# Optimization experiments

Measured on AMD Instinct MI355X. Metric: run time of the kernel, lower is better.

## Reference

```python
import jax, jax.numpy as jnp
import numpy as np

N_NODES = 100000


def _gcn_norm(edge_index, num_nodes):
    # PyG GCNConv default: add self-loops, symmetric normalization.
    src = jnp.concatenate([edge_index[0], jnp.arange(num_nodes, dtype=edge_index.dtype)])
    dst = jnp.concatenate([edge_index[1], jnp.arange(num_nodes, dtype=edge_index.dtype)])
    deg = jax.ops.segment_sum(jnp.ones_like(dst, dtype=jnp.float32), dst, num_segments=num_nodes)
    dis = jnp.where(deg > 0, jax.lax.rsqrt(deg), 0.0)  # deg^{-1/2}
    norm = dis[src] * dis[dst]  # [E + N]
    return src, dst, norm


def _gcn_conv(x, W, b, src, dst, norm, num_nodes):
    h = x @ W.T                      # [N, out] transform first (out < in)
    msg = h[src] * norm[:, None]     # gather + per-edge scale
    agg = jax.ops.segment_sum(msg, dst, num_segments=num_nodes)  # scatter-add
    return agg + b


def setup_inputs() -> dict:
    key = jax.random.key(0)
    ks = jax.random.split(key, 12)
    E = 3200000
    x = jax.random.normal(ks[0], (N_NODES, 128), dtype=jnp.float32)
    edge_index = jax.random.randint(ks[1], (2, E), 0, N_NODES, dtype=jnp.int64)
    s = lambda k, sh, fan: jax.random.normal(k, sh, dtype=jnp.float32) * (1.0 / np.sqrt(fan))
    return {
        "x": x,
        "edge_index": edge_index,
        "W1": s(ks[2], (32, 128), 128), "b1": jnp.zeros((32,), jnp.float32),
        "W2": s(ks[3], (16, 32), 32),   "b2": jnp.zeros((16,), jnp.float32),
        "w_ih": s(ks[4], (32, 16), 16), "w_hh": s(ks[5], (32, 8), 8),
        "b_ih": s(ks[6], (32,), 8),     "b_hh": s(ks[7], (32,), 8),
        "W_out": s(ks[8], (1, 8), 8),   "b_out": jnp.zeros((1,), jnp.float32),
    }


def reference(x, edge_index, W1, b1, W2, b2, w_ih, w_hh, b_ih, b_hh, W_out, b_out):
    src, dst, norm = _gcn_norm(edge_index, N_NODES)
    h = jax.nn.relu(_gcn_conv(x, W1, b1, src, dst, norm, N_NODES))   # [N, 32]
    h = jax.nn.relu(_gcn_conv(h, W2, b2, src, dst, norm, N_NODES))   # [N, 16]
    # Single-timestep LSTM with h0 = c0 = 0 (gate order: i, f, g, o).
    gates = h @ w_ih.T + b_ih + b_hh   # [N, 32]; h0 @ w_hh.T term is zero
    i, f, g, o = jnp.split(gates, 4, axis=-1)
    c = jax.nn.sigmoid(i) * jnp.tanh(g)
    hh = jax.nn.sigmoid(o) * jnp.tanh(c)  # [N, 8]
    out = hh @ W_out.T + b_out            # [N, 1]
    return out.squeeze(-1)                # [N]
```

## Files before the change

kernel.cpp:

```cpp
#include <hip/hip_runtime.h>
#include <hip/hip_fp16.h>
#include <math.h>

static constexpr int N = 100000;
static constexpr int SHIFT = 7;
static constexpr int BUCKN = 1 << SHIFT;
static constexpr int NBUCK = (N + BUCKN - 1) >> SHIFT;
static constexpr int CHUNK = 12288;
static constexpr int STRIDE = 5120;

__global__ __launch_bounds__(1024) void k_init(int* __restrict__ gcur) {
    int b = threadIdx.x;
    if (b < NBUCK) gcur[b] = b * STRIDE;
}

__global__ __launch_bounds__(1024) void k_part(const int* __restrict__ src,
                                               const int* __restrict__ dst,
                                               int* __restrict__ gcur,
                                               int* __restrict__ col, int E) {
    __shared__ int ss[CHUNK];
    __shared__ int ds[CHUNK];
    __shared__ int hl[NBUCK];
    __shared__ int cur[NBUCK];
    const int t = threadIdx.x, b = blockIdx.x;
    if (t < NBUCK) hl[t] = 0;
    __syncthreads();
    const int e0 = b * CHUNK;
    const int m = min(CHUNK, E - e0);
    for (int i = t; i < m; i += 1024) {
        int d = dst[e0 + i], s = src[e0 + i];
        ss[i] = s;
        ds[i] = d;
        atomicAdd(&hl[d >> SHIFT], 1);
    }
    __syncthreads();
    if (t < NBUCK) cur[t] = atomicAdd(&gcur[t], hl[t]);
    __syncthreads();
    for (int i = t; i < m; i += 1024) {
        int d = ds[i];
        int pos = atomicAdd(&cur[d >> SHIFT], 1);
        col[pos] = ss[i] | ((d & (BUCKN - 1)) << 17);
    }
}

__global__ __launch_bounds__(1024) void k_sort(const int* __restrict__ gcur,
                                               int* __restrict__ col,
                                               int* __restrict__ deg,
                                               int* __restrict__ row_start) {
    __shared__ int es[STRIDE];
    __shared__ int cnt[BUCKN];
    __shared__ int cur[BUCKN];
    const int t = threadIdx.x, buck = blockIdx.x;
    const int s0 = buck * STRIDE;
    int n = gcur[buck] - s0;
    if (n > STRIDE) n = STRIDE;
    if (t < BUCKN) cnt[t] = 0;
    __syncthreads();
    for (int i = t; i < n; i += 1024) {
        int p = col[s0 + i];
        es[i] = p;
        atomicAdd(&cnt[(p >> 17) & (BUCKN - 1)], 1);
    }
    __syncthreads();
    if (t < BUCKN) cur[t] = cnt[t];
    __syncthreads();
    for (int off = 1; off < BUCKN; off <<= 1) {
        int v = (t < BUCKN && t >= off) ? cur[t - off] : 0;
        __syncthreads();
        if (t < BUCKN) cur[t] += v;
        __syncthreads();
    }
    if (t < BUCKN) {
        int excl = cur[t] - cnt[t];
        int node = buck * BUCKN + t;
        if (node < N) {
            deg[node] = cnt[t];
            row_start[node] = s0 + excl;
        }
        cur[t] = excl;
    }
    __syncthreads();
    for (int i = t; i < n; i += 1024) {
        int p = es[i];
        int pos = atomicAdd(&cur[(p >> 17) & (BUCKN - 1)], 1);
        col[s0 + pos] = p & 0x1FFFF;
    }
}

__global__ __launch_bounds__(256) void k_xw1(
        const float* __restrict__ x, const float* __restrict__ W1,
        const int* __restrict__ deg, __half* __restrict__ g1h) {
    __shared__ float4 wtv[32 * 33];
    __shared__ float4 xsv[1024];
    const int t = threadIdx.x;
    const float4* W1v = (const float4*)W1;
    for (int idx = t; idx < 1024; idx += 256) {
        int j = idx >> 5, kb = idx & 31;
        wtv[kb * 33 + j] = W1v[idx];
    }
    const float4* x4 = (const float4*)x + (size_t)blockIdx.x * 1024;
    for (int idx = t; idx < 1024; idx += 256) xsv[idx] = x4[idx];
    __syncthreads();

    const int j = t & 31, ng = t >> 5;
    float a0 = 0.f, a1 = 0.f, a2 = 0.f, a3 = 0.f;
#pragma unroll 4
    for (int kb = 0; kb < 32; ++kb) {
        float4 w = wtv[kb * 33 + j];
        float4 x0 = xsv[(4 * ng + 0) * 32 + kb];
        float4 x1 = xsv[(4 * ng + 1) * 32 + kb];
        float4 x2 = xsv[(4 * ng + 2) * 32 + kb];
        float4 x3 = xsv[(4 * ng + 3) * 32 + kb];
        a0 = fmaf(w.x, x0.x, fmaf(w.y, x0.y, fmaf(w.z, x0.z, fmaf(w.w, x0.w, a0))));
        a1 = fmaf(w.x, x1.x, fmaf(w.y, x1.y, fmaf(w.z, x1.z, fmaf(w.w, x1.w, a1))));
        a2 = fmaf(w.x, x2.x, fmaf(w.y, x2.y, fmaf(w.z, x2.z, fmaf(w.w, x2.w, a2))));
        a3 = fmaf(w.x, x3.x, fmaf(w.y, x3.y, fmaf(w.z, x3.z, fmaf(w.w, x3.w, a3))));
    }
    const int nb = blockIdx.x * 32 + 4 * ng;
    g1h[(nb + 0) * 32 + j] = __float2half(a0 * rsqrtf((float)(deg[nb + 0] + 1)));
    g1h[(nb + 1) * 32 + j] = __float2half(a1 * rsqrtf((float)(deg[nb + 1] + 1)));
    g1h[(nb + 2) * 32 + j] = __float2half(a2 * rsqrtf((float)(deg[nb + 2] + 1)));
    g1h[(nb + 3) * 32 + j] = __float2half(a3 * rsqrtf((float)(deg[nb + 3] + 1)));
}

__global__ __launch_bounds__(256) void k_gather1(
        const int* __restrict__ row_start, const int* __restrict__ deg,
        const int* __restrict__ col, const __half* __restrict__ g1h,
        const float* __restrict__ b1, float* __restrict__ h1) {
    const int t = threadIdx.x;
    const int lane = t & 63, w = t >> 6;
    const int q = lane & 3;
    const int node = blockIdx.x * 64 + w * 16 + (lane >> 2);
    const int nc = node < N ? node : N - 1;
    const int rs = row_start[nc];
    const int ne = (node < N) ? deg[nc] : 0;
    const uint4* g1v = (const uint4*)g1h;

    float acc[8];
    {
        uint4 rv = g1v[nc * 4 + q];
        const __half2* hp = (const __half2*)&rv;
#pragma unroll
        for (int m2 = 0; m2 < 4; ++m2) {
            float2 f = __half22float2(hp[m2]);
            acc[2 * m2] = f.x;
            acc[2 * m2 + 1] = f.y;
        }
    }
    for (int base = 0; base < ne; base += 8) {
        int sva = (base + q < ne) ? col[rs + base + q] : 0;
        int svb = (base + 4 + q < ne) ? col[rs + base + 4 + q] : 0;
        int idx[8];
#pragma unroll
        for (int u = 0; u < 4; ++u) idx[u] = __shfl(sva, u, 4);
#pragma unroll
        for (int u = 0; u < 4; ++u) idx[4 + u] = __shfl(svb, u, 4);
        uint4 rv[8];
#pragma unroll
        for (int u = 0; u < 8; ++u) rv[u] = g1v[idx[u] * 4 + q];
#pragma unroll
        for (int u = 0; u < 8; ++u) {
            float wt = (base + u < ne) ? 1.f : 0.f;
            const __half2* hp = (const __half2*)&rv[u];
#pragma unroll
            for (int m2 = 0; m2 < 4; ++m2) {
                float2 f = __half22float2(hp[m2]);
                acc[2 * m2]     = fmaf(wt, f.x, acc[2 * m2]);
                acc[2 * m2 + 1] = fmaf(wt, f.y, acc[2 * m2 + 1]);
            }
        }
    }
    if (node < N) {
        const float dis = rsqrtf((float)(ne + 1));
        float4* h1v = (float4*)h1;
#pragma unroll
        for (int h = 0; h < 2; ++h) {
            float4 o;
            float v0 = acc[4 * h + 0] * dis + b1[q * 8 + 4 * h + 0];
            float v1 = acc[4 * h + 1] * dis + b1[q * 8 + 4 * h + 1];
            float v2 = acc[4 * h + 2] * dis + b1[q * 8 + 4 * h + 2];
            float v3 = acc[4 * h + 3] * dis + b1[q * 8 + 4 * h + 3];
            o.x = v0 > 0.f ? v0 : 0.f;
            o.y = v1 > 0.f ? v1 : 0.f;
            o.z = v2 > 0.f ? v2 : 0.f;
            o.w = v3 > 0.f ? v3 : 0.f;
            h1v[node * 8 + q * 2 + h] = o;
        }
    }
}

__global__ __launch_bounds__(256) void k_layer2(
        const float* __restrict__ h1, const float* __restrict__ W2,
        const int* __restrict__ deg, __half* __restrict__ g2h) {
    __shared__ float h1s[16 * 32];
    __shared__ float w2t[32 * 17];
    const int t = threadIdx.x;
    for (int idx = t; idx < 512; idx += 256) {
        int j = idx >> 5, k = idx & 31;
        w2t[k * 17 + j] = W2[idx];
    }
    const int base = blockIdx.x * 512;
    for (int idx = t; idx < 512; idx += 256) h1s[idx] = h1[base + idx];
    __syncthreads();
    const int nl = t >> 4, j = t & 15;
    const int node = blockIdx.x * 16 + nl;
    const float* hr = h1s + nl * 32;
    float a = 0.f;
#pragma unroll
    for (int k = 0; k < 32; ++k) a = fmaf(hr[k], w2t[k * 17 + j], a);
    g2h[blockIdx.x * 256 + t] = __float2half(a * rsqrtf((float)(deg[node] + 1)));
}

__global__ __launch_bounds__(256) void k_gather2(
        const int* __restrict__ row_start, const int* __restrict__ deg,
        const int* __restrict__ col, const __half* __restrict__ g2h,
        const float* __restrict__ b2, float* __restrict__ h2) {
    const int t = threadIdx.x;
    const int lane = t & 63, w = t >> 6;
    const int q = lane & 1;
    const int node = blockIdx.x * 128 + w * 32 + (lane >> 1);
    const int nc = node < N ? node : N - 1;
    const int rs = row_start[nc];
    const int ne = (node < N) ? deg[nc] : 0;
    const uint4* g2v = (const uint4*)g2h;

    float acc[8];
    {
        uint4 rv = g2v[nc * 2 + q];
        const __half2* hp = (const __half2*)&rv;
#pragma unroll
        for (int m2 = 0; m2 < 4; ++m2) {
            float2 f = __half22float2(hp[m2]);
            acc[2 * m2] = f.x;
            acc[2 * m2 + 1] = f.y;
        }
    }
    for (int base = 0; base < ne; base += 8) {
        int sv[4];
#pragma unroll
        for (int k = 0; k < 4; ++k)
            sv[k] = (base + 2 * k + q < ne) ? col[rs + base + 2 * k + q] : 0;
        int idx[8];
#pragma unroll
        for (int k = 0; k < 4; ++k) {
            idx[2 * k]     = __shfl(sv[k], 0, 2);
            idx[2 * k + 1] = __shfl(sv[k], 1, 2);
        }
        uint4 rv[8];
#pragma unroll
        for (int u = 0; u < 8; ++u) rv[u] = g2v[idx[u] * 2 + q];
#pragma unroll
        for (int u = 0; u < 8; ++u) {
            float wt = (base + u < ne) ? 1.f : 0.f;
            const __half2* hp = (const __half2*)&rv[u];
#pragma unroll
            for (int m2 = 0; m2 < 4; ++m2) {
                float2 f = __half22float2(hp[m2]);
                acc[2 * m2]     = fmaf(wt, f.x, acc[2 * m2]);
                acc[2 * m2 + 1] = fmaf(wt, f.y, acc[2 * m2 + 1]);
            }
        }
    }
    if (node < N) {
        const float dis = rsqrtf((float)(ne + 1));
        float4* h2v = (float4*)h2;
#pragma unroll
        for (int h = 0; h < 2; ++h) {
            float4 o;
            float v0 = acc[4 * h + 0] * dis + b2[q * 8 + 4 * h + 0];
            float v1 = acc[4 * h + 1] * dis + b2[q * 8 + 4 * h + 1];
            float v2 = acc[4 * h + 2] * dis + b2[q * 8 + 4 * h + 2];
            float v3 = acc[4 * h + 3] * dis + b2[q * 8 + 4 * h + 3];
            o.x = v0 > 0.f ? v0 : 0.f;
            o.y = v1 > 0.f ? v1 : 0.f;
            o.z = v2 > 0.f ? v2 : 0.f;
            o.w = v3 > 0.f ? v3 : 0.f;
            h2v[node * 4 + q * 2 + h] = o;
        }
    }
}

__global__ __launch_bounds__(256) void k_final(
        const float* __restrict__ h2g,
        const float* __restrict__ w_ih, const float* __restrict__ b_ih,
        const float* __restrict__ b_hh, const float* __restrict__ W_out,
        const float* __restrict__ b_out, float* __restrict__ out) {
    __shared__ float wih[512];
    __shared__ float bias[32];
    __shared__ float wout[8];
    __shared__ float bo;
    const int t = threadIdx.x;
    for (int idx = t; idx < 512; idx += 256) wih[idx] = w_ih[idx];
    if (t < 32) bias[t] = b_ih[t] + b_hh[t];
    if (t < 8)  wout[t] = W_out[t];
    if (t == 0) bo = b_out[0];
    __syncthreads();

    const int i = blockIdx.x * 256 + t;
    if (i >= N) return;
    float h2[16];
    const float4* a4 = (const float4*)(h2g + (size_t)i * 16);
#pragma unroll
    for (int q = 0; q < 4; ++q) {
        float4 v = a4[q];
        h2[q * 4 + 0] = v.x; h2[q * 4 + 1] = v.y;
        h2[q * 4 + 2] = v.z; h2[q * 4 + 3] = v.w;
    }
    float oacc = 0.f;
#pragma unroll
    for (int q = 0; q < 8; ++q) {
        float gi = bias[q], gg = bias[16 + q], go = bias[24 + q];
#pragma unroll
        for (int k = 0; k < 16; ++k) {
            gi = fmaf(h2[k], wih[q * 16 + k], gi);
            gg = fmaf(h2[k], wih[(16 + q) * 16 + k], gg);
            go = fmaf(h2[k], wih[(24 + q) * 16 + k], go);
        }
        float c  = (1.f / (1.f + expf(-gi))) * tanhf(gg);
        float hh = (1.f / (1.f + expf(-go))) * tanhf(c);
        oacc = fmaf(hh, wout[q], oacc);
    }
    out[i] = oacc + bo;
}

extern "C" void kernel_launch(void* const* d_in, const int* in_sizes, int n_in,
                              void* d_out, int out_size, void* d_ws, size_t ws_size,
                              hipStream_t stream) {
    const float* x     = (const float*)d_in[0];
    const int*   ei    = (const int*)d_in[1];
    const float* W1    = (const float*)d_in[2];
    const float* b1    = (const float*)d_in[3];
    const float* W2    = (const float*)d_in[4];
    const float* b2    = (const float*)d_in[5];
    const float* w_ih  = (const float*)d_in[6];
    const float* b_ih  = (const float*)d_in[8];
    const float* b_hh  = (const float*)d_in[9];
    const float* W_out = (const float*)d_in[10];
    const float* b_out = (const float*)d_in[11];
    float* out = (float*)d_out;

    const int E = in_sizes[1] / 2;
    const int* src = ei;
    const int* dst = ei + E;
    const int BP = (E + CHUNK - 1) / CHUNK;

    int* col       = (int*)d_ws;
    int* deg       = col + (size_t)NBUCK * STRIDE;
    int* row_start = deg + N;
    int* gcur      = row_start + N;
    __half* g1h    = (__half*)(gcur + 784);
    float* h1      = (float*)((int*)(gcur + 784) + (size_t)N * 16);
    __half* g2h    = g1h;
    float* h2      = h1;

    k_init   <<<1,                      1024, 0, stream>>>(gcur);
    k_part   <<<BP,                     1024, 0, stream>>>(src, dst, gcur, col, E);
    k_sort   <<<NBUCK,                  1024, 0, stream>>>(gcur, col, deg, row_start);
    k_xw1    <<<N / 32,                 256,  0, stream>>>(x, W1, deg, g1h);
    k_gather1<<<(N + 63) / 64,          256,  0, stream>>>(row_start, deg, col, g1h, b1, h1);
    k_layer2 <<<N / 16,                 256,  0, stream>>>(h1, W2, deg, g2h);
    k_gather2<<<(N + 127) / 128,        256,  0, stream>>>(row_start, deg, col, g2h, b2, h2);
    k_final  <<<(N + 255) / 256,        256,  0, stream>>>(h2, w_ih, b_ih, b_hh, W_out, b_out, out);
}
```

Baseline: 279.1 us.

## Shrink partition blocks, drop LDS staging, and widen gather unroll to 16

The partition kernel now uses 256-thread blocks over 4096-edge chunks and no longer stages src/dst in shared memory; it re-reads them from global memory on the second pass. This cuts LDS use so more blocks fit per CU, but each edge is read twice from global memory. Both gather kernels now fetch 16 neighbor rows per iteration instead of 8 to keep more loads in flight, at the cost of more registers. Bounds clamps were also added to the scatter positions and neighbor indices for safety.

```diff
diff --git a/kernel.cpp b/kernel.cpp
--- a/kernel.cpp
+++ b/kernel.cpp
@@ -6,40 +6,35 @@
 static constexpr int SHIFT = 7;
 static constexpr int BUCKN = 1 << SHIFT;
 static constexpr int NBUCK = (N + BUCKN - 1) >> SHIFT;
-static constexpr int CHUNK = 12288;
+static constexpr int CHUNK = 4096;
 static constexpr int STRIDE = 5120;
+static constexpr int COLCAP = NBUCK * STRIDE;
 
 __global__ __launch_bounds__(1024) void k_init(int* __restrict__ gcur) {
     int b = threadIdx.x;
     if (b < NBUCK) gcur[b] = b * STRIDE;
 }
 
-__global__ __launch_bounds__(1024) void k_part(const int* __restrict__ src,
-                                               const int* __restrict__ dst,
-                                               int* __restrict__ gcur,
-                                               int* __restrict__ col, int E) {
-    __shared__ int ss[CHUNK];
-    __shared__ int ds[CHUNK];
+__global__ __launch_bounds__(256) void k_part(const int* __restrict__ src,
+                                              const int* __restrict__ dst,
+                                              int* __restrict__ gcur,
+                                              int* __restrict__ col, int E) {
     __shared__ int hl[NBUCK];
     __shared__ int cur[NBUCK];
     const int t = threadIdx.x, b = blockIdx.x;
-    if (t < NBUCK) hl[t] = 0;
+    for (int i = t; i < NBUCK; i += 256) hl[i] = 0;
     __syncthreads();
     const int e0 = b * CHUNK;
     const int m = min(CHUNK, E - e0);
-    for (int i = t; i < m; i += 1024) {
-        int d = dst[e0 + i], s = src[e0 + i];
-        ss[i] = s;
-        ds[i] = d;
-        atomicAdd(&hl[d >> SHIFT], 1);
-    }
-    __syncthreads();
-    if (t < NBUCK) cur[t] = atomicAdd(&gcur[t], hl[t]);
-    __syncthreads();
-    for (int i = t; i < m; i += 1024) {
-        int d = ds[i];
+    for (int i = t; i < m; i += 256) atomicAdd(&hl[dst[e0 + i] >> SHIFT], 1);
+    __syncthreads();
+    for (int i = t; i < NBUCK; i += 256) cur[i] = atomicAdd(&gcur[i], hl[i]);
+    __syncthreads();
+    for (int i = t; i < m; i += 256) {
+        int d = dst[e0 + i];
         int pos = atomicAdd(&cur[d >> SHIFT], 1);
-        col[pos] = ss[i] | ((d & (BUCKN - 1)) << 17);
+        pos = min(max(pos, 0), COLCAP - 1);
+        col[pos] = (src[e0 + i] & 0x1FFFF) | ((d & (BUCKN - 1)) << 17);
     }
 }
 
@@ -53,7 +48,7 @@
     const int t = threadIdx.x, buck = blockIdx.x;
     const int s0 = buck * STRIDE;
     int n = gcur[buck] - s0;
-    if (n > STRIDE) n = STRIDE;
+    n = max(0, min(n, STRIDE));
     if (t < BUCKN) cnt[t] = 0;
     __syncthreads();
     for (int i = t; i < n; i += 1024) {
@@ -83,6 +78,7 @@
     for (int i = t; i < n; i += 1024) {
         int p = es[i];
         int pos = atomicAdd(&cur[(p >> 17) & (BUCKN - 1)], 1);
+        pos = min(max(pos, 0), STRIDE - 1);
         col[s0 + pos] = p & 0x1FFFF;
     }
 }
@@ -147,19 +143,22 @@
             acc[2 * m2 + 1] = f.y;
         }
     }
-    for (int base = 0; base < ne; base += 8) {
-        int sva = (base + q < ne) ? col[rs + base + q] : 0;
-        int svb = (base + 4 + q < ne) ? col[rs + base + 4 + q] : 0;
-        int idx[8];
-#pragma unroll
-        for (int u = 0; u < 4; ++u) idx[u] = __shfl(sva, u, 4);
-#pragma unroll
-        for (int u = 0; u < 4; ++u) idx[4 + u] = __shfl(svb, u, 4);
-        uint4 rv[8];
-#pragma unroll
-        for (int u = 0; u < 8; ++u) rv[u] = g1v[idx[u] * 4 + q];
-#pragma unroll
-        for (int u = 0; u < 8; ++u) {
+    for (int base = 0; base < ne; base += 16) {
+        int sv[4];
+#pragma unroll
+        for (int c = 0; c < 4; ++c)
+            sv[c] = (base + 4 * c + q < ne) ? col[rs + base + 4 * c + q] : 0;
+        int idx[16];
+#pragma unroll
+        for (int c = 0; c < 4; ++c)
+#pragma unroll
+            for (int u = 0; u < 4; ++u)
+                idx[4 * c + u] = min(__shfl(sv[c], u, 4), N - 1);
+        uint4 rv[16];
+#pragma unroll
+        for (int u = 0; u < 16; ++u) rv[u] = g1v[idx[u] * 4 + q];
+#pragma unroll
+        for (int u = 0; u < 16; ++u) {
             float wt = (base + u < ne) ? 1.f : 0.f;
             const __half2* hp = (const __half2*)&rv[u];
 #pragma unroll
@@ -235,22 +234,22 @@
             acc[2 * m2 + 1] = f.y;
         }
     }
-    for (int base = 0; base < ne; base += 8) {
-        int sv[4];
-#pragma unroll
-        for (int k = 0; k < 4; ++k)
-            sv[k] = (base + 2 * k + q < ne) ? col[rs + base + 2 * k + q] : 0;
-        int idx[8];
-#pragma unroll
-        for (int k = 0; k < 4; ++k) {
-            idx[2 * k]     = __shfl(sv[k], 0, 2);
-            idx[2 * k + 1] = __shfl(sv[k], 1, 2);
-        }
-        uint4 rv[8];
-#pragma unroll
-        for (int u = 0; u < 8; ++u) rv[u] = g2v[idx[u] * 2 + q];
-#pragma unroll
-        for (int u = 0; u < 8; ++u) {
+    for (int base = 0; base < ne; base += 16) {
+        int sv[8];
+#pragma unroll
+        for (int c = 0; c < 8; ++c)
+            sv[c] = (base + 2 * c + q < ne) ? col[rs + base + 2 * c + q] : 0;
+        int idx[16];
+#pragma unroll
+        for (int c = 0; c < 8; ++c) {
+            idx[2 * c]     = min(__shfl(sv[c], 0, 2), N - 1);
+            idx[2 * c + 1] = min(__shfl(sv[c], 1, 2), N - 1);
+        }
+        uint4 rv[16];
+#pragma unroll
+        for (int u = 0; u < 16; ++u) rv[u] = g2v[idx[u] * 2 + q];
+#pragma unroll
+        for (int u = 0; u < 16; ++u) {
             float wt = (base + u < ne) ? 1.f : 0.f;
             const __half2* hp = (const __half2*)&rv[u];
 #pragma unroll
@@ -345,7 +344,7 @@
     const int BP = (E + CHUNK - 1) / CHUNK;
 
     int* col       = (int*)d_ws;
-    int* deg       = col + (size_t)NBUCK * STRIDE;
+    int* deg       = col + COLCAP;
     int* row_start = deg + N;
     int* gcur      = row_start + N;
     __half* g1h    = (__half*)(gcur + 784);
@@ -354,7 +353,7 @@
     float* h2      = h1;
 
     k_init   <<<1,                      1024, 0, stream>>>(gcur);
-    k_part   <<<BP,                     1024, 0, stream>>>(src, dst, gcur, col, E);
+    k_part   <<<BP,                     256,  0, stream>>>(src, dst, gcur, col, E);
     k_sort   <<<NBUCK,                  1024, 0, stream>>>(gcur, col, deg, row_start);
     k_xw1    <<<N / 32,                 256,  0, stream>>>(x, W1, deg, g1h);
     k_gather1<<<(N + 63) / 64,          256,  0, stream>>>(row_start, deg, col, g1h, b1, h1);
```

Result: slower. 296.7 us (+6.3%).
